# Performance work log

Measured on AMD Instinct MI355X. Metric: run time of the kernel, lower is better.

The kernel has to match this reference:

```python
import jax, jax.numpy as jnp
import numpy as np
from jax import lax

B = 32768        # batch
L = 1024         # input_size
K = 5            # kernel_size
PAD = K - 1      # circular padding = 4
FEA = L + (PAD - K // 2) * 2   # mem_fea_dim = 1028
MEM_DIM = 50
DATE_DIM = 32
SHRINK = 0.0025
EPS = 1e-12
DN = ('NCH', 'OIH', 'NCH')


def setup_inputs() -> dict:
    key = jax.random.key(0)
    ks = jax.random.split(key, 10)
    s = 0.05
    return {
        'x': jax.random.normal(ks[0], (B, L), jnp.float32),
        'date_vector': jax.random.normal(ks[1], (B, DATE_DIM), jnp.float32),
        'conv_w': jax.random.normal(ks[2], (1, 1, K), jnp.float32) * s,    # Conv1d weight [out,in,k]
        'convt_w': jax.random.normal(ks[3], (1, 1, K), jnp.float32) * s,   # ConvTranspose1d weight
        'mem_W': jax.random.normal(ks[4], (MEM_DIM, FEA), jnp.float32) * s,      # memory bank (codebook)
        'date_W': jax.random.normal(ks[5], (MEM_DIM, DATE_DIM), jnp.float32) * s, # date addressing weights
        'fcw_w': jax.random.normal(ks[6], (1, L), jnp.float32) * s,
        'fcw_b': jnp.zeros((1,), jnp.float32),
        'fcb_w': jax.random.normal(ks[7], (1, L), jnp.float32) * s,
        'fcb_b': jnp.zeros((1,), jnp.float32),
    }


def _forward(x, date_vector, conv_w, convt_w, mem_W, date_W, fcw_w, fcw_b, fcb_w, fcb_b):
    # --- encode: 1-channel circular conv (bias forced to 0 in original forward) ---
    st = x[:, None, :]                                            # [B,1,L]
    stp = jnp.pad(st, ((0, 0), (0, 0), (PAD, PAD)), mode='wrap')  # circular pad
    st = lax.conv_general_dilated(stp, conv_w, (1,), 'VALID', dimension_numbers=DN)  # [B,1,FEA]

    # --- DateMemoryUnit: date-addressed read with hard shrink + L1 renorm ---
    scores = date_vector @ date_W.T                               # [B,MEM_DIM]
    att = jax.nn.softmax(scores, axis=-1)
    att = jax.nn.relu(att - SHRINK) * att / (jnp.abs(att - SHRINK) + EPS)
    att = att / (jnp.sum(jnp.abs(att), axis=-1, keepdims=True) + EPS)
    st_mem = att @ mem_W                                          # [B,FEA]
    st = st_mem.reshape(B, 1, FEA)

    # --- decode: ConvTranspose1d(k=5, stride=1, padding=4) == VALID conv with flipped kernel ---
    st = lax.conv_general_dilated(st, jnp.flip(convt_w, -1), (1,), 'VALID', dimension_numbers=DN)
    st = st[:, 0, :]                                              # [B,L]

    # --- trend blend ---
    mtf = 0.5
    weight = jnp.tanh(x @ fcw_w.T + fcw_b) * mtf + 1.0            # [B,1]
    bias = jnp.tanh(x @ fcb_w.T + fcb_b) * mtf                    # [B,1]
    st = st * weight + bias
    return st, weight, bias


def reference(x, date_vector, conv_w, convt_w, mem_W, date_W, fcw_w, fcw_b, fcb_w, fcb_b):
    return _forward(x, date_vector, conv_w, convt_w, mem_W, date_W, fcw_w, fcw_b, fcb_w, fcb_b)
```

## Files before the change

kernel.cpp:

```cpp
#include <hip/hip_runtime.h>
#include <hip/hip_bf16.h>

#define BB   32768
#define LL   1024
#define FEA  1028
#define MEM  50
#define DATE 32

typedef float  f32x4  __attribute__((ext_vector_type(4)));
typedef __bf16 bf16x8 __attribute__((ext_vector_type(8)));

__device__ __forceinline__ float wave_max(float v) {
    #pragma unroll
    for (int off = 32; off; off >>= 1) v = fmaxf(v, __shfl_xor(v, off));
    return v;
}
__device__ __forceinline__ float wave_sum(float v) {
    #pragma unroll
    for (int off = 32; off; off >>= 1) v += __shfl_xor(v, off);
    return v;
}

__global__ void prep_wc(const float* __restrict__ convt_w,
                        const float* __restrict__ mem_W,
                        __bf16* __restrict__ wc) {
    int idx = blockIdx.x * 256 + threadIdx.x;
    int n = idx >> 6, k = idx & 63;
    float acc = 0.f;
    if (k < MEM) {
        #pragma unroll
        for (int j = 0; j < 5; ++j)
            acc += convt_w[j] * mem_W[k * FEA + n + 4 - j];
    }
    wc[n * 64 + k] = (__bf16)acc;
}

__global__ __launch_bounds__(256) void memconv_fused(
        const float* __restrict__ x,
        const float* __restrict__ dv,
        const float* __restrict__ dW,
        const float* __restrict__ fcw_w, const float* __restrict__ fcw_b,
        const float* __restrict__ fcb_w, const float* __restrict__ fcb_b,
        const __bf16* __restrict__ wc,
        float* __restrict__ out) {
    __shared__ __bf16 att_s[16 * 72];
    __shared__ float  w_s[16], b_s[16];
    __shared__ float  stage[4][16 * 72];

    const int lane = threadIdx.x & 63;
    const int wid  = threadIdx.x >> 6;
    const int cg   = lane & 15;
    const int kg   = lane >> 4;
    const int b0   = blockIdx.x * 16;

    {
        int m = lane < MEM ? lane : MEM - 1;
        float dwv[DATE];
        const f32x4* dwp = (const f32x4*)(dW + m * DATE);
        #pragma unroll
        for (int c = 0; c < 8; ++c) {
            f32x4 v = dwp[c];
            #pragma unroll
            for (int j = 0; j < 4; ++j) dwv[c * 4 + j] = v[j];
        }
        #pragma unroll
        for (int rr = 0; rr < 4; ++rr) {
            int r = wid * 4 + rr;
            const f32x4* dvp = (const f32x4*)(dv + (size_t)(b0 + r) * DATE);
            float sc = 0.f;
            #pragma unroll
            for (int c = 0; c < 8; ++c) {
                f32x4 v = dvp[c];
                #pragma unroll
                for (int j = 0; j < 4; ++j) sc += v[j] * dwv[c * 4 + j];
            }
            float scm = (lane < MEM) ? sc : -1e30f;
            float mx  = wave_max(scm);
            float e   = (lane < MEM) ? __expf(sc - mx) : 0.f;
            float s   = wave_sum(e);
            float p   = e / s;
            float d   = p - 0.0025f;
            float p2  = (d > 0.f) ? p * d / (d + 1e-12f) : 0.f;
            float s2  = wave_sum(p2) + 1e-12f;
            float att = p2 / s2;
            att_s[r * 72 + lane] = (lane < MEM) ? (__bf16)att : (__bf16)0.f;
        }
    }

    {
        f32x4 wv[4], bv[4];
        #pragma unroll
        for (int c = 0; c < 4; ++c) {
            wv[c] = *(const f32x4*)(fcw_w + c * 256 + lane * 4);
            bv[c] = *(const f32x4*)(fcb_w + c * 256 + lane * 4);
        }
        f32x4 xv[4][4];
        #pragma unroll
        for (int rr = 0; rr < 4; ++rr)
            #pragma unroll
            for (int c = 0; c < 4; ++c)
                xv[rr][c] = *(const f32x4*)(x + (size_t)(b0 + wid * 4 + rr) * LL
                                              + c * 256 + lane * 4);
        #pragma unroll
        for (int rr = 0; rr < 4; ++rr) {
            int r = wid * 4 + rr;
            float aw = 0.f, ab = 0.f;
            #pragma unroll
            for (int c = 0; c < 4; ++c)
                #pragma unroll
                for (int j = 0; j < 4; ++j) {
                    aw += xv[rr][c][j] * wv[c][j];
                    ab += xv[rr][c][j] * bv[c][j];
                }
            #pragma unroll
            for (int off = 1; off <= 32; off <<= 1) {
                aw += __shfl_xor(aw, off);
                ab += __shfl_xor(ab, off);
            }
            float w  = tanhf(aw + fcw_b[0]) * 0.5f + 1.0f;
            float bi = tanhf(ab + fcb_b[0]) * 0.5f;
            if (lane == 0) {
                w_s[r] = w; b_s[r] = bi;
                out[(size_t)BB * LL + (b0 + r)]      = w;
                out[(size_t)BB * LL + BB + (b0 + r)] = bi;
            }
        }
    }
    __syncthreads();

    {
        bf16x8 bfr0 = *(const bf16x8*)(att_s + cg * 72 + kg * 8);
        bf16x8 bfr1 = *(const bf16x8*)(att_s + cg * 72 + 32 + kg * 8);
        float* st = stage[wid];
        const int n0 = wid * 256;
        #pragma unroll
        for (int R = 0; R < 4; ++R) {
            #pragma unroll
            for (int t = 0; t < 4; ++t) {
                int n = n0 + (R * 4 + t) * 16 + cg;
                bf16x8 a0 = *(const bf16x8*)(wc + n * 64 + kg * 8);
                bf16x8 a1 = *(const bf16x8*)(wc + n * 64 + 32 + kg * 8);
                f32x4 acc = {0.f, 0.f, 0.f, 0.f};
                acc = __builtin_amdgcn_mfma_f32_16x16x32_bf16(a0, bfr0, acc, 0, 0, 0);
                acc = __builtin_amdgcn_mfma_f32_16x16x32_bf16(a1, bfr1, acc, 0, 0, 0);
                *(f32x4*)(st + cg * 72 + t * 16 + kg * 4) = acc;
            }
            #pragma unroll
            for (int j = 0; j < 4; ++j) {
                int row = j * 4 + (lane >> 4);
                int nl  = (lane & 15) * 4;
                f32x4 v = *(const f32x4*)(st + row * 72 + nl);
                float w = w_s[row], bi = b_s[row];
                f32x4 o;
                #pragma unroll
                for (int k = 0; k < 4; ++k) o[k] = v[k] * w + bi;
                *(f32x4*)(out + (size_t)(b0 + row) * LL + n0 + R * 64 + nl) = o;
            }
        }
    }
}

extern "C" void kernel_launch(void* const* d_in, const int* in_sizes, int n_in,
                              void* d_out, int out_size, void* d_ws, size_t ws_size,
                              hipStream_t stream) {
    const float* x     = (const float*)d_in[0];
    const float* dv    = (const float*)d_in[1];
    const float* convt = (const float*)d_in[3];
    const float* memW  = (const float*)d_in[4];
    const float* dateW = (const float*)d_in[5];
    const float* fcww  = (const float*)d_in[6];
    const float* fcwb  = (const float*)d_in[7];
    const float* fcbw  = (const float*)d_in[8];
    const float* fcbb  = (const float*)d_in[9];
    float* out = (float*)d_out;
    __bf16* wc = (__bf16*)d_ws;

    prep_wc      <<<256,     256, 0, stream>>>(convt, memW, wc);
    memconv_fused<<<BB / 16, 256, 0, stream>>>(x, dv, dateW, fcww, fcwb, fcbw, fcbb, wc, out);
}
```

Before: 274.8 us.

## Split weight/bias reduction into prep kernel and use nontemporal output stores

Moves the x-row dot products and tanh for the trend weight and bias out of the main kernel and into the prep kernel, which also builds the combined conv/memory matrix. The main kernel then reads weight and bias back from the output buffer, so it no longer loads x and carries less register pressure. The main output stores become nontemporal and tanh is replaced by an exp-based formula. The risk is that the separate kernel still reads all of x, while the handoff adds a global-memory round trip for weight and bias, plus one more block-scheduling phase.

```diff
diff --git a/kernel.cpp b/kernel.cpp
--- a/kernel.cpp
+++ b/kernel.cpp
@@ -20,27 +20,76 @@
     for (int off = 32; off; off >>= 1) v += __shfl_xor(v, off);
     return v;
 }
-
-__global__ void prep_wc(const float* __restrict__ convt_w,
-                        const float* __restrict__ mem_W,
-                        __bf16* __restrict__ wc) {
-    int idx = blockIdx.x * 256 + threadIdx.x;
-    int n = idx >> 6, k = idx & 63;
-    float acc = 0.f;
-    if (k < MEM) {
-        #pragma unroll
-        for (int j = 0; j < 5; ++j)
-            acc += convt_w[j] * mem_W[k * FEA + n + 4 - j];
-    }
-    wc[n * 64 + k] = (__bf16)acc;
+__device__ __forceinline__ float fast_tanh(float v) {
+    float e = __expf(2.f * v);
+    return 1.f - 2.f / (e + 1.f);
 }
 
-__global__ __launch_bounds__(256) void memconv_fused(
+__global__ __launch_bounds__(256) void prep_and_wb(
+        const float* __restrict__ convt_w,
+        const float* __restrict__ mem_W,
         const float* __restrict__ x,
+        const float* __restrict__ fcw_w, const float* __restrict__ fcw_b,
+        const float* __restrict__ fcb_w, const float* __restrict__ fcb_b,
+        __bf16* __restrict__ wc,
+        float* __restrict__ out) {
+    if (blockIdx.x >= 2048) {
+        int idx = (blockIdx.x - 2048) * 256 + threadIdx.x;
+        int n = idx >> 6, k = idx & 63;
+        float acc = 0.f;
+        if (k < MEM) {
+            #pragma unroll
+            for (int j = 0; j < 5; ++j)
+                acc += convt_w[j] * mem_W[k * FEA + n + 4 - j];
+        }
+        wc[n * 64 + k] = (__bf16)acc;
+        return;
+    }
+
+    const int lane = threadIdx.x & 63;
+    const int wid  = threadIdx.x >> 6;
+    const int b0   = blockIdx.x * 16;
+
+    f32x4 wv[4], bv[4];
+    #pragma unroll
+    for (int c = 0; c < 4; ++c) {
+        wv[c] = *(const f32x4*)(fcw_w + c * 256 + lane * 4);
+        bv[c] = *(const f32x4*)(fcb_w + c * 256 + lane * 4);
+    }
+    f32x4 xv[4][4];
+    #pragma unroll
+    for (int rr = 0; rr < 4; ++rr)
+        #pragma unroll
+        for (int c = 0; c < 4; ++c)
+            xv[rr][c] = *(const f32x4*)(x + (size_t)(b0 + wid * 4 + rr) * LL
+                                          + c * 256 + lane * 4);
+    float fwb = fcw_b[0], fbb = fcb_b[0];
+    #pragma unroll
+    for (int rr = 0; rr < 4; ++rr) {
+        int r = wid * 4 + rr;
+        float aw = 0.f, ab = 0.f;
+        #pragma unroll
+        for (int c = 0; c < 4; ++c)
+            #pragma unroll
+            for (int j = 0; j < 4; ++j) {
+                aw += xv[rr][c][j] * wv[c][j];
+                ab += xv[rr][c][j] * bv[c][j];
+            }
+        #pragma unroll
+        for (int off = 1; off <= 32; off <<= 1) {
+            aw += __shfl_xor(aw, off);
+            ab += __shfl_xor(ab, off);
+        }
+        if (lane == 0) {
+            out[(size_t)BB * LL + (b0 + r)]      = fast_tanh(aw + fwb) * 0.5f + 1.0f;
+            out[(size_t)BB * LL + BB + (b0 + r)] = fast_tanh(ab + fbb) * 0.5f;
+        }
+    }
+}
+
+__global__ __launch_bounds__(256) void memconv_main(
         const float* __restrict__ dv,
         const float* __restrict__ dW,
-        const float* __restrict__ fcw_w, const float* __restrict__ fcw_b,
-        const float* __restrict__ fcb_w, const float* __restrict__ fcb_b,
         const __bf16* __restrict__ wc,
         float* __restrict__ out) {
     __shared__ __bf16 att_s[16 * 72];
@@ -52,6 +101,11 @@
     const int cg   = lane & 15;
     const int kg   = lane >> 4;
     const int b0   = blockIdx.x * 16;
+
+    if (threadIdx.x < 16) {
+        w_s[threadIdx.x] = out[(size_t)BB * LL + b0 + threadIdx.x];
+        b_s[threadIdx.x] = out[(size_t)BB * LL + BB + b0 + threadIdx.x];
+    }
 
     {
         int m = lane < MEM ? lane : MEM - 1;
@@ -86,46 +140,6 @@
             att_s[r * 72 + lane] = (lane < MEM) ? (__bf16)att : (__bf16)0.f;
         }
     }
-
-    {
-        f32x4 wv[4], bv[4];
-        #pragma unroll
-        for (int c = 0; c < 4; ++c) {
-            wv[c] = *(const f32x4*)(fcw_w + c * 256 + lane * 4);
-            bv[c] = *(const f32x4*)(fcb_w + c * 256 + lane * 4);
-        }
-        f32x4 xv[4][4];
-        #pragma unroll
-        for (int rr = 0; rr < 4; ++rr)
-            #pragma unroll
-            for (int c = 0; c < 4; ++c)
-                xv[rr][c] = *(const f32x4*)(x + (size_t)(b0 + wid * 4 + rr) * LL
-                                              + c * 256 + lane * 4);
-        #pragma unroll
-        for (int rr = 0; rr < 4; ++rr) {
-            int r = wid * 4 + rr;
-            float aw = 0.f, ab = 0.f;
-            #pragma unroll
-            for (int c = 0; c < 4; ++c)
-                #pragma unroll
-                for (int j = 0; j < 4; ++j) {
-                    aw += xv[rr][c][j] * wv[c][j];
-                    ab += xv[rr][c][j] * bv[c][j];
-                }
-            #pragma unroll
-            for (int off = 1; off <= 32; off <<= 1) {
-                aw += __shfl_xor(aw, off);
-                ab += __shfl_xor(ab, off);
-            }
-            float w  = tanhf(aw + fcw_b[0]) * 0.5f + 1.0f;
-            float bi = tanhf(ab + fcb_b[0]) * 0.5f;
-            if (lane == 0) {
-                w_s[r] = w; b_s[r] = bi;
-                out[(size_t)BB * LL + (b0 + r)]      = w;
-                out[(size_t)BB * LL + BB + (b0 + r)] = bi;
-            }
-        }
-    }
     __syncthreads();
 
     {
@@ -154,7 +168,8 @@
                 f32x4 o;
                 #pragma unroll
                 for (int k = 0; k < 4; ++k) o[k] = v[k] * w + bi;
-                *(f32x4*)(out + (size_t)(b0 + row) * LL + n0 + R * 64 + nl) = o;
+                __builtin_nontemporal_store(
+                    o, (f32x4*)(out + (size_t)(b0 + row) * LL + n0 + R * 64 + nl));
             }
         }
     }
@@ -175,6 +190,6 @@
     float* out = (float*)d_out;
     __bf16* wc = (__bf16*)d_ws;
 
-    prep_wc      <<<256,     256, 0, stream>>>(convt, memW, wc);
-    memconv_fused<<<BB / 16, 256, 0, stream>>>(x, dv, dateW, fcww, fcwb, fcbw, fcbb, wc, out);
+    prep_and_wb <<<2304,    256, 0, stream>>>(convt, memW, x, fcww, fcwb, fcbw, fcbb, wc, out);
+    memconv_main<<<BB / 16, 256, 0, stream>>>(dv, dateW, wc, out);
 }
```

After: 287.5 us. 1.05x slower.

## Overlap x loads with softmax, batch wave reductions, drop max, use fast tanh

Applied to the files above, without the earlier changes.

Half of the x rows are now loaded before the date-attention softmax and the other half right after it, so global-load latency overlaps the attention math. The four rows' shuffle reductions are interleaved to expose independent work, and the softmax max-subtraction is removed. tanhf is replaced by an exp-based approximation, and the launch bounds now request 2 blocks per SM. Dropping the max subtraction risks exp overflow for large scores, and the occupancy hint may force register spills.

```diff
diff --git a/kernel.cpp b/kernel.cpp
--- a/kernel.cpp
+++ b/kernel.cpp
@@ -10,20 +10,15 @@
 typedef float  f32x4  __attribute__((ext_vector_type(4)));
 typedef __bf16 bf16x8 __attribute__((ext_vector_type(8)));
 
-__device__ __forceinline__ float wave_max(float v) {
-    #pragma unroll
-    for (int off = 32; off; off >>= 1) v = fmaxf(v, __shfl_xor(v, off));
-    return v;
-}
-__device__ __forceinline__ float wave_sum(float v) {
-    #pragma unroll
-    for (int off = 32; off; off >>= 1) v += __shfl_xor(v, off);
-    return v;
-}
-
-__global__ void prep_wc(const float* __restrict__ convt_w,
-                        const float* __restrict__ mem_W,
-                        __bf16* __restrict__ wc) {
+__device__ __forceinline__ float fast_tanh(float v) {
+    float e = __expf(2.f * v);
+    return 1.f - 2.f / (e + 1.f);
+}
+
+__global__ __launch_bounds__(256) void prep_wc(
+        const float* __restrict__ convt_w,
+        const float* __restrict__ mem_W,
+        __bf16* __restrict__ wc) {
     int idx = blockIdx.x * 256 + threadIdx.x;
     int n = idx >> 6, k = idx & 63;
     float acc = 0.f;
@@ -35,7 +30,7 @@
     wc[n * 64 + k] = (__bf16)acc;
 }
 
-__global__ __launch_bounds__(256) void memconv_fused(
+__global__ __launch_bounds__(256, 2) void memconv_fused2(
         const float* __restrict__ x,
         const float* __restrict__ dv,
         const float* __restrict__ dW,
@@ -53,6 +48,20 @@
     const int kg   = lane >> 4;
     const int b0   = blockIdx.x * 16;
 
+    f32x4 wv[4], bv[4];
+    #pragma unroll
+    for (int c = 0; c < 4; ++c) {
+        wv[c] = *(const f32x4*)(fcw_w + c * 256 + lane * 4);
+        bv[c] = *(const f32x4*)(fcb_w + c * 256 + lane * 4);
+    }
+    f32x4 xv0[2][4];
+    #pragma unroll
+    for (int rr = 0; rr < 2; ++rr)
+        #pragma unroll
+        for (int c = 0; c < 4; ++c)
+            xv0[rr][c] = *(const f32x4*)(x + (size_t)(b0 + wid * 4 + rr) * LL
+                                           + c * 256 + lane * 4);
+
     {
         int m = lane < MEM ? lane : MEM - 1;
         float dwv[DATE];
@@ -63,10 +72,10 @@
             #pragma unroll
             for (int j = 0; j < 4; ++j) dwv[c * 4 + j] = v[j];
         }
+        float e[4];
         #pragma unroll
         for (int rr = 0; rr < 4; ++rr) {
-            int r = wid * 4 + rr;
-            const f32x4* dvp = (const f32x4*)(dv + (size_t)(b0 + r) * DATE);
+            const f32x4* dvp = (const f32x4*)(dv + (size_t)(b0 + wid * 4 + rr) * DATE);
             float sc = 0.f;
             #pragma unroll
             for (int c = 0; c < 8; ++c) {
@@ -74,52 +83,83 @@
                 #pragma unroll
                 for (int j = 0; j < 4; ++j) sc += v[j] * dwv[c * 4 + j];
             }
-            float scm = (lane < MEM) ? sc : -1e30f;
-            float mx  = wave_max(scm);
-            float e   = (lane < MEM) ? __expf(sc - mx) : 0.f;
-            float s   = wave_sum(e);
-            float p   = e / s;
-            float d   = p - 0.0025f;
-            float p2  = (d > 0.f) ? p * d / (d + 1e-12f) : 0.f;
-            float s2  = wave_sum(p2) + 1e-12f;
-            float att = p2 / s2;
-            att_s[r * 72 + lane] = (lane < MEM) ? (__bf16)att : (__bf16)0.f;
-        }
-    }
+            e[rr] = (lane < MEM) ? __expf(sc) : 0.f;
+        }
+        float s[4] = {e[0], e[1], e[2], e[3]};
+        #pragma unroll
+        for (int off = 32; off; off >>= 1) {
+            #pragma unroll
+            for (int rr = 0; rr < 4; ++rr) s[rr] += __shfl_xor(s[rr], off);
+        }
+        float p2[4];
+        #pragma unroll
+        for (int rr = 0; rr < 4; ++rr) {
+            float p = e[rr] / s[rr];
+            float d = p - 0.0025f;
+            p2[rr]  = (d > 0.f) ? p * d / (d + 1e-12f) : 0.f;
+        }
+        float s2[4] = {p2[0], p2[1], p2[2], p2[3]};
+        #pragma unroll
+        for (int off = 32; off; off >>= 1) {
+            #pragma unroll
+            for (int rr = 0; rr < 4; ++rr) s2[rr] += __shfl_xor(s2[rr], off);
+        }
+        #pragma unroll
+        for (int rr = 0; rr < 4; ++rr) {
+            float att = p2[rr] / (s2[rr] + 1e-12f);
+            att_s[(wid * 4 + rr) * 72 + lane] = (lane < MEM) ? (__bf16)att : (__bf16)0.f;
+        }
+    }
+
+    f32x4 xv1[2][4];
+    #pragma unroll
+    for (int rr = 0; rr < 2; ++rr)
+        #pragma unroll
+        for (int c = 0; c < 4; ++c)
+            xv1[rr][c] = *(const f32x4*)(x + (size_t)(b0 + wid * 4 + 2 + rr) * LL
+                                           + c * 256 + lane * 4);
 
     {
-        f32x4 wv[4], bv[4];
-        #pragma unroll
-        for (int c = 0; c < 4; ++c) {
-            wv[c] = *(const f32x4*)(fcw_w + c * 256 + lane * 4);
-            bv[c] = *(const f32x4*)(fcb_w + c * 256 + lane * 4);
-        }
-        f32x4 xv[4][4];
-        #pragma unroll
-        for (int rr = 0; rr < 4; ++rr)
+        float aw[4], ab[4];
+        #pragma unroll
+        for (int rr = 0; rr < 2; ++rr) {
+            float sa = 0.f, sb = 0.f;
             #pragma unroll
             for (int c = 0; c < 4; ++c)
-                xv[rr][c] = *(const f32x4*)(x + (size_t)(b0 + wid * 4 + rr) * LL
-                                              + c * 256 + lane * 4);
-        #pragma unroll
-        for (int rr = 0; rr < 4; ++rr) {
-            int r = wid * 4 + rr;
-            float aw = 0.f, ab = 0.f;
+                #pragma unroll
+                for (int j = 0; j < 4; ++j) {
+                    sa += xv0[rr][c][j] * wv[c][j];
+                    sb += xv0[rr][c][j] * bv[c][j];
+                }
+            aw[rr] = sa; ab[rr] = sb;
+        }
+        #pragma unroll
+        for (int rr = 0; rr < 2; ++rr) {
+            float sa = 0.f, sb = 0.f;
             #pragma unroll
             for (int c = 0; c < 4; ++c)
                 #pragma unroll
                 for (int j = 0; j < 4; ++j) {
-                    aw += xv[rr][c][j] * wv[c][j];
-                    ab += xv[rr][c][j] * bv[c][j];
+                    sa += xv1[rr][c][j] * wv[c][j];
+                    sb += xv1[rr][c][j] * bv[c][j];
                 }
-            #pragma unroll
-            for (int off = 1; off <= 32; off <<= 1) {
-                aw += __shfl_xor(aw, off);
-                ab += __shfl_xor(ab, off);
-            }
-            float w  = tanhf(aw + fcw_b[0]) * 0.5f + 1.0f;
-            float bi = tanhf(ab + fcb_b[0]) * 0.5f;
-            if (lane == 0) {
+            aw[2 + rr] = sa; ab[2 + rr] = sb;
+        }
+        #pragma unroll
+        for (int off = 1; off <= 32; off <<= 1) {
+            #pragma unroll
+            for (int rr = 0; rr < 4; ++rr) {
+                aw[rr] += __shfl_xor(aw[rr], off);
+                ab[rr] += __shfl_xor(ab[rr], off);
+            }
+        }
+        if (lane == 0) {
+            float fwb = fcw_b[0], fbb = fcb_b[0];
+            #pragma unroll
+            for (int rr = 0; rr < 4; ++rr) {
+                int r = wid * 4 + rr;
+                float w  = fast_tanh(aw[rr] + fwb) * 0.5f + 1.0f;
+                float bi = fast_tanh(ab[rr] + fbb) * 0.5f;
                 w_s[r] = w; b_s[r] = bi;
                 out[(size_t)BB * LL + (b0 + r)]      = w;
                 out[(size_t)BB * LL + BB + (b0 + r)] = bi;
@@ -175,6 +215,6 @@
     float* out = (float*)d_out;
     __bf16* wc = (__bf16*)d_ws;
 
-    prep_wc      <<<256,     256, 0, stream>>>(convt, memW, wc);
-    memconv_fused<<<BB / 16, 256, 0, stream>>>(x, dv, dateW, fcww, fcwb, fcbw, fcbb, wc, out);
-}
+    prep_wc       <<<256,     256, 0, stream>>>(convt, memW, wc);
+    memconv_fused2<<<BB / 16, 256, 0, stream>>>(x, dv, dateW, fcww, fcwb, fcbw, fcbb, wc, out);
+}
```

Result: no change. 273.2 us (-0.6%).
